# Kernel optimization log

Measured on AMD Instinct MI355X. Metric: run time of the kernel, lower is better.

The kernel has to match this reference:

```python
import jax, jax.numpy as jnp
import numpy as np

C = 512      # input/value channels
DK = 64      # key/query channels (C // 8, SAGAN convention)
N = 4096     # flattened spatial positions (64x64)


def setup_inputs() -> dict:
    key = jax.random.key(0)
    k1, k2, k3, k4 = jax.random.split(key, 4)
    x = jax.random.normal(k1, (C, N), dtype=jnp.float32)
    # 1x1 conv projections == linear maps over the channel dim
    Wk = jax.random.normal(k2, (DK, C), dtype=jnp.float32) * (1.0 / np.sqrt(C))
    Wq = jax.random.normal(k3, (DK, C), dtype=jnp.float32) * (1.0 / np.sqrt(C))
    Wv = jax.random.normal(k4, (C, C), dtype=jnp.float32) * (1.0 / np.sqrt(C))
    return {"x": x, "Wk": Wk, "Wq": Wq, "Wv": Wv}


def reference(x, Wk, Wq, Wv):
    # conv 1x1 projections: [dk, N] / [dk, N] / [C, N]
    kx = Wk @ x
    qx = Wq @ x
    vx = Wv @ x
    # alpha_{i,j} = softmax_j( f(x_i)^T g(x_j) )  -> [N, N]
    scores = jnp.einsum('di,dj->ij', kx, qx)
    attn = jax.nn.softmax(scores, axis=-1)
    # o_i = sum_j alpha_{i,j} h(x_j)  -> [N, C]
    out = attn @ vx.T
    return out
```

## Files before the change

### kernel.cpp

```cpp
#include <hip/hip_runtime.h>
#include <hip/hip_bf16.h>

typedef __bf16 bf16x8 __attribute__((ext_vector_type(8)));
typedef float f32x4 __attribute__((ext_vector_type(4)));
typedef unsigned int u32x4 __attribute__((ext_vector_type(4)));

#define MFMA16(a, b, c) __builtin_amdgcn_mfma_f32_16x16x32_bf16((a), (b), (c), 0, 0, 0)
#define DEVI static __device__ __forceinline__

DEVI unsigned short f2bf(float f) {
  union { float f; unsigned u; } x; x.f = f;
  unsigned r = x.u + 0x7fffu + ((x.u >> 16) & 1u);
  return (unsigned short)(r >> 16);
}
DEVI float bf2f(unsigned short h) {
  union { unsigned u; float f; } x; x.u = ((unsigned)h) << 16;
  return x.f;
}
DEVI bf16x8 ld16(const void* p) {
  u32x4 t = *reinterpret_cast<const u32x4*>(p);
  return __builtin_bit_cast(bf16x8, t);
}

__global__ __launch_bounds__(256) void prep_kernel(
    const float* __restrict__ x,
    const float* __restrict__ Wk, const float* __restrict__ Wq, const float* __restrict__ Wv,
    unsigned short* __restrict__ xThi, unsigned short* __restrict__ xTlo,
    unsigned short* __restrict__ Wkhi, unsigned short* __restrict__ Wklo,
    unsigned short* __restrict__ Wqhi, unsigned short* __restrict__ Wqlo,
    unsigned short* __restrict__ Wvhi, unsigned short* __restrict__ Wvlo) {
  __shared__ float xs[64][65];
  const int bid = blockIdx.x;
  const int t = threadIdx.x;
  if (bid < 512) {
    const int c0 = (bid & 7) * 64, j0 = (bid >> 3) * 64;
    {
      const int cr = t >> 2, jc = (t & 3) * 16;
      const float4* s4 = reinterpret_cast<const float4*>(x + (size_t)(c0 + cr) * 4096 + j0 + jc);
#pragma unroll
      for (int q = 0; q < 4; ++q) {
        float4 v = s4[q];
        xs[cr][jc + q * 4 + 0] = v.x;
        xs[cr][jc + q * 4 + 1] = v.y;
        xs[cr][jc + q * 4 + 2] = v.z;
        xs[cr][jc + q * 4 + 3] = v.w;
      }
    }
    __syncthreads();
    {
      const int jr = t >> 2, cs = (t & 3) * 16;
      unsigned short hb[16] __attribute__((aligned(16)));
      unsigned short lb[16] __attribute__((aligned(16)));
#pragma unroll
      for (int u = 0; u < 16; ++u) {
        float v = xs[cs + u][jr];
        unsigned short h = f2bf(v);
        hb[u] = h;
        lb[u] = f2bf(v - bf2f(h));
      }
      unsigned short* dh = xThi + (size_t)(j0 + jr) * 512 + c0 + cs;
      unsigned short* dl = xTlo + (size_t)(j0 + jr) * 512 + c0 + cs;
      reinterpret_cast<u32x4*>(dh)[0] = reinterpret_cast<const u32x4*>(hb)[0];
      reinterpret_cast<u32x4*>(dh)[1] = reinterpret_cast<const u32x4*>(hb)[1];
      reinterpret_cast<u32x4*>(dl)[0] = reinterpret_cast<const u32x4*>(lb)[0];
      reinterpret_cast<u32x4*>(dl)[1] = reinterpret_cast<const u32x4*>(lb)[1];
    }
  } else {
    const int nk = 64 * 512 / 4, nv = 512 * 512 / 4;
    int i = (bid - 512) * 256 + t;
    const float* in; unsigned short* hi; unsigned short* lo; int idx;
    if (i < nk)               { in = Wk; hi = Wkhi; lo = Wklo; idx = i; }
    else if (i < 2 * nk)      { in = Wq; hi = Wqhi; lo = Wqlo; idx = i - nk; }
    else if (i < 2 * nk + nv) { in = Wv; hi = Wvhi; lo = Wvlo; idx = i - 2 * nk; }
    else return;
    float4 v = reinterpret_cast<const float4*>(in)[idx];
    float vv[4] = {v.x, v.y, v.z, v.w};
    unsigned short hb[4] __attribute__((aligned(8)));
    unsigned short lb[4] __attribute__((aligned(8)));
#pragma unroll
    for (int e = 0; e < 4; ++e) { hb[e] = f2bf(vv[e]); lb[e] = f2bf(vv[e] - bf2f(hb[e])); }
    reinterpret_cast<uint2*>(hi)[idx] = *reinterpret_cast<const uint2*>(hb);
    reinterpret_cast<uint2*>(lo)[idx] = *reinterpret_cast<const uint2*>(lb);
  }
}

__global__ __launch_bounds__(256) void proj_kernel(
    const unsigned short* __restrict__ Wkhi, const unsigned short* __restrict__ Wklo,
    const unsigned short* __restrict__ Wqhi, const unsigned short* __restrict__ Wqlo,
    const unsigned short* __restrict__ Wvhi, const unsigned short* __restrict__ Wvlo,
    const unsigned short* __restrict__ xThi, const unsigned short* __restrict__ xTlo,
    unsigned short* __restrict__ kxThi, unsigned short* __restrict__ kxTlo,
    unsigned short* __restrict__ qxThi, unsigned short* __restrict__ qxTlo,
    unsigned short* __restrict__ vbf) {
  const int y = blockIdx.y;
  const int w = threadIdx.x >> 6, lane = threadIdx.x & 63;
  const int li = lane & 15, g = lane >> 4;
  if (y < 8) {
    const int j0 = blockIdx.x * 64 + (w >> 1) * 32;
    const int c0 = y * 64 + (w & 1) * 32;
    f32x4 acc[2][2];
#pragma unroll
    for (int mf = 0; mf < 2; ++mf)
#pragma unroll
      for (int nf = 0; nf < 2; ++nf) acc[mf][nf] = f32x4{0.f, 0.f, 0.f, 0.f};
    for (int kf = 0; kf < 16; ++kf) {
      const int kk = kf * 32 + g * 8;
      bf16x8 ah[2], al[2], bh[2], bl[2];
#pragma unroll
      for (int mf = 0; mf < 2; ++mf) {
        ah[mf] = ld16(xThi + (size_t)(j0 + mf * 16 + li) * 512 + kk);
        al[mf] = ld16(xTlo + (size_t)(j0 + mf * 16 + li) * 512 + kk);
      }
#pragma unroll
      for (int nf = 0; nf < 2; ++nf) {
        bh[nf] = ld16(Wvhi + (size_t)(c0 + nf * 16 + li) * 512 + kk);
        bl[nf] = ld16(Wvlo + (size_t)(c0 + nf * 16 + li) * 512 + kk);
      }
#pragma unroll
      for (int mf = 0; mf < 2; ++mf)
#pragma unroll
        for (int nf = 0; nf < 2; ++nf) {
          acc[mf][nf] = MFMA16(ah[mf], bh[nf], acc[mf][nf]);
          acc[mf][nf] = MFMA16(ah[mf], bl[nf], acc[mf][nf]);
          acc[mf][nf] = MFMA16(al[mf], bh[nf], acc[mf][nf]);
        }
    }
#pragma unroll
    for (int mf = 0; mf < 2; ++mf)
#pragma unroll
      for (int nf = 0; nf < 2; ++nf) {
        unsigned short hv[4] __attribute__((aligned(8)));
#pragma unroll
        for (int r = 0; r < 4; ++r) hv[r] = f2bf(acc[mf][nf][r]);
        *reinterpret_cast<uint2*>(vbf + (size_t)(c0 + nf * 16 + li) * 4096 + j0 + mf * 16 + g * 4) =
            *reinterpret_cast<const uint2*>(hv);
      }
  } else {
    const int mb = y - 8;
    const int j0 = blockIdx.x * 64 + w * 16;
    const unsigned short* Whi = (mb < 4 ? Wkhi : Wqhi) + (size_t)((mb & 3) * 16 + li) * 512 + g * 8;
    const unsigned short* Wlo = (mb < 4 ? Wklo : Wqlo) + (size_t)((mb & 3) * 16 + li) * 512 + g * 8;
    const unsigned short* Xh = xThi + (size_t)(j0 + li) * 512 + g * 8;
    const unsigned short* Xl = xTlo + (size_t)(j0 + li) * 512 + g * 8;
    f32x4 acc = f32x4{0.f, 0.f, 0.f, 0.f};
    for (int kf = 0; kf < 16; ++kf) {
      const int o = kf * 32;
      bf16x8 ah = ld16(Whi + o), al = ld16(Wlo + o);
      bf16x8 bh = ld16(Xh + o), bl = ld16(Xl + o);
      acc = MFMA16(ah, bh, acc);
      acc = MFMA16(ah, bl, acc);
      acc = MFMA16(al, bh, acc);
    }
    unsigned short hv[4] __attribute__((aligned(8))), lv[4] __attribute__((aligned(8)));
#pragma unroll
    for (int r = 0; r < 4; ++r) {
      hv[r] = f2bf(acc[r]);
      lv[r] = f2bf(acc[r] - bf2f(hv[r]));
    }
    unsigned short* oh = (mb < 4 ? kxThi : qxThi) + (size_t)(j0 + li) * 64 + (mb & 3) * 16 + g * 4;
    unsigned short* ol = (mb < 4 ? kxTlo : qxTlo) + (size_t)(j0 + li) * 64 + (mb & 3) * 16 + g * 4;
    *reinterpret_cast<uint2*>(oh) = *reinterpret_cast<const uint2*>(hv);
    *reinterpret_cast<uint2*>(ol) = *reinterpret_cast<const uint2*>(lv);
  }
}

__global__ __launch_bounds__(256, 2) void attn_kernel(
    const unsigned short* __restrict__ kxThi, const unsigned short* __restrict__ kxTlo,
    const unsigned short* __restrict__ qxThi, const unsigned short* __restrict__ qxTlo,
    const unsigned short* __restrict__ vbf,
    unsigned short* __restrict__ pacc, float* __restrict__ pml, int split) {
  __shared__ __align__(16) unsigned short PL[4096];
  __shared__ __align__(16) float smax[64][4];
  __shared__ __align__(16) float ssum[64][4];
  const int jchunk = 4096 / split;
  const int s = blockIdx.x % split;
  const int i0 = (blockIdx.x / split) * 64;
  const int jbase = s * jchunk;
  const int w = threadIdx.x >> 6, lane = threadIdx.x & 63;
  const int li = lane & 15, g = lane >> 4;
  const float L2E = 1.4426950408889634f;
  char* plb = reinterpret_cast<char*>(PL);

  bf16x8 qh[4][2], ql[4][2];
#pragma unroll
  for (int f = 0; f < 4; ++f)
#pragma unroll
    for (int kf = 0; kf < 2; ++kf) {
      const size_t o = (size_t)(i0 + f * 16 + li) * 64 + kf * 32 + g * 8;
      qh[f][kf] = ld16(kxThi + o);
      ql[f][kf] = ld16(kxTlo + o);
    }
  f32x4 acc[8][4];
#pragma unroll
  for (int cf = 0; cf < 8; ++cf)
#pragma unroll
    for (int f = 0; f < 4; ++f) acc[cf][f] = f32x4{0.f, 0.f, 0.f, 0.f};
  float m_run[4] = {-3.0e38f, -3.0e38f, -3.0e38f, -3.0e38f};
  float l_run[4] = {0.f, 0.f, 0.f, 0.f};

  for (int jj = 0; jj < jchunk; jj += 64) {
    const int j0 = jbase + jj;
    f32x4 sc[4];
#pragma unroll
    for (int f = 0; f < 4; ++f) sc[f] = f32x4{0.f, 0.f, 0.f, 0.f};
    {
      const unsigned short* ah_p = qxThi + (size_t)(j0 + w * 16 + li) * 64 + g * 8;
      const unsigned short* al_p = qxTlo + (size_t)(j0 + w * 16 + li) * 64 + g * 8;
#pragma unroll
      for (int kf = 0; kf < 2; ++kf) {
        bf16x8 ah = ld16(ah_p + kf * 32);
        bf16x8 al = ld16(al_p + kf * 32);
#pragma unroll
        for (int f = 0; f < 4; ++f) {
          sc[f] = MFMA16(ah, qh[f][kf], sc[f]);
          sc[f] = MFMA16(ah, ql[f][kf], sc[f]);
          sc[f] = MFMA16(al, qh[f][kf], sc[f]);
        }
      }
    }
    {
      float pm[4];
#pragma unroll
      for (int f = 0; f < 4; ++f) {
        float tm = fmaxf(fmaxf(sc[f][0], sc[f][1]), fmaxf(sc[f][2], sc[f][3]));
        tm = fmaxf(tm, __shfl_xor(tm, 16));
        tm = fmaxf(tm, __shfl_xor(tm, 32));
        pm[f] = tm;
      }
      if (lane < 16) {
#pragma unroll
        for (int f = 0; f < 4; ++f) smax[f * 16 + li][w] = pm[f];
      }
    }
    __syncthreads();
    float fac[4];
#pragma unroll
    for (int f = 0; f < 4; ++f) {
      const f32x4 sm = *reinterpret_cast<const f32x4*>(&smax[f * 16 + li][0]);
      const float m_new = fmaxf(fmaxf(sm[0], sm[1]), fmaxf(sm[2], sm[3]));
      fac[f] = 1.0f;
      if (m_new > m_run[f] + 8.0f) {
        fac[f] = exp2f((m_run[f] - m_new) * L2E);
        m_run[f] = m_new;
#pragma unroll
        for (int cf = 0; cf < 8; ++cf) {
#pragma unroll
          for (int r = 0; r < 4; ++r) acc[cf][f][r] *= fac[f];
        }
      }
    }
#pragma unroll
    for (int f = 0; f < 4; ++f) {
      float p[4];
#pragma unroll
      for (int r = 0; r < 4; ++r) p[r] = exp2f((sc[f][r] - m_run[f]) * L2E);
      float ps = (p[0] + p[1]) + (p[2] + p[3]);
      ps += __shfl_xor(ps, 16);
      ps += __shfl_xor(ps, 32);
      if (lane < 16) ssum[f * 16 + li][w] = ps;
      unsigned short pv[4] __attribute__((aligned(8)));
#pragma unroll
      for (int r = 0; r < 4; ++r) pv[r] = f2bf(p[r]);
      const int pb = ((f * 16 + li) * 128 + w * 32 + g * 8) ^ ((li & 7) << 4);
      *reinterpret_cast<uint2*>(plb + pb) = *reinterpret_cast<const uint2*>(pv);
    }
    __syncthreads();
#pragma unroll
    for (int f = 0; f < 4; ++f) {
      const f32x4 ss = *reinterpret_cast<const f32x4*>(&ssum[f * 16 + li][0]);
      l_run[f] = l_run[f] * fac[f] + ((ss[0] + ss[1]) + (ss[2] + ss[3]));
    }
    bf16x8 bp[4][2];
#pragma unroll
    for (int f = 0; f < 4; ++f)
#pragma unroll
      for (int kf = 0; kf < 2; ++kf) {
        const int rb = ((f * 16 + li) * 128 + kf * 64 + g * 16) ^ ((li & 7) << 4);
        bp[f][kf] = ld16(plb + rb);
      }
#pragma unroll
    for (int cf = 0; cf < 8; ++cf) {
      const unsigned short* vp = vbf + (size_t)(w * 128 + cf * 16 + li) * 4096 + j0 + g * 8;
      bf16x8 a0 = ld16(vp);
      bf16x8 a1 = ld16(vp + 32);
#pragma unroll
      for (int f = 0; f < 4; ++f) {
        acc[cf][f] = MFMA16(a0, bp[f][0], acc[cf][f]);
        acc[cf][f] = MFMA16(a1, bp[f][1], acc[cf][f]);
      }
    }
  }
#pragma unroll
  for (int cf = 0; cf < 8; ++cf)
#pragma unroll
    for (int f = 0; f < 4; ++f) {
      unsigned short hv[4] __attribute__((aligned(8)));
#pragma unroll
      for (int r = 0; r < 4; ++r) hv[r] = f2bf(acc[cf][f][r]);
      unsigned short* dp = pacc + ((size_t)(s * 4096 + i0 + f * 16 + li)) * 512 + w * 128 + cf * 16 + g * 4;
      *reinterpret_cast<uint2*>(dp) = *reinterpret_cast<const uint2*>(hv);
    }
  if (w == 0 && lane < 16) {
#pragma unroll
    for (int f = 0; f < 4; ++f) {
      pml[((size_t)(s * 4096 + i0 + f * 16 + li)) * 2] = m_run[f];
      pml[((size_t)(s * 4096 + i0 + f * 16 + li)) * 2 + 1] = l_run[f];
    }
  }
}

__global__ __launch_bounds__(256) void combine_kernel(
    const unsigned short* __restrict__ pacc, const float* __restrict__ pml,
    float* __restrict__ out, int split) {
  const int t = blockIdx.x * 256 + threadIdx.x;
  const int i = t >> 6, c8 = (t & 63) << 3;
  const float L2E = 1.4426950408889634f;
  float M = -3.0e38f;
  for (int ss = 0; ss < split; ++ss) M = fmaxf(M, pml[((size_t)ss * 4096 + i) * 2]);
  float num[8];
#pragma unroll
  for (int e = 0; e < 8; ++e) num[e] = 0.f;
  float den = 0.f;
  for (int ss = 0; ss < split; ++ss) {
    const float m = pml[((size_t)ss * 4096 + i) * 2];
    const float l = pml[((size_t)ss * 4096 + i) * 2 + 1];
    const float wgt = exp2f((m - M) * L2E);
    den += wgt * l;
    u32x4 pk = *reinterpret_cast<const u32x4*>(pacc + ((size_t)ss * 4096 + i) * 512 + c8);
#pragma unroll
    for (int e = 0; e < 8; ++e) {
      unsigned short h = (unsigned short)((pk[e >> 1] >> ((e & 1) * 16)) & 0xffffu);
      num[e] += wgt * bf2f(h);
    }
  }
  const float inv = 1.0f / den;
  float4 o0, o1;
  o0.x = num[0] * inv; o0.y = num[1] * inv; o0.z = num[2] * inv; o0.w = num[3] * inv;
  o1.x = num[4] * inv; o1.y = num[5] * inv; o1.z = num[6] * inv; o1.w = num[7] * inv;
  float* op = out + (size_t)i * 512 + c8;
  *reinterpret_cast<float4*>(op) = o0;
  *reinterpret_cast<float4*>(op + 4) = o1;
}

extern "C" void kernel_launch(void* const* d_in, const int* in_sizes, int n_in,
                              void* d_out, int out_size, void* d_ws, size_t ws_size,
                              hipStream_t stream) {
  const float* x  = (const float*)d_in[0];
  const float* Wk = (const float*)d_in[1];
  const float* Wq = (const float*)d_in[2];
  const float* Wv = (const float*)d_in[3];
  float* out = (float*)d_out;
  char* ws = (char*)d_ws;

  const size_t MB = 1024ull * 1024ull;
  const size_t pers_b = 2 * MB  + 4 * MB ;
  int split = 8;
  {
    size_t need8 = (size_t)8 * 4 * MB + 8 * 4096 * 8 + pers_b;
    if (ws_size < need8) split = 4;
  }
  const size_t pacc_b = (size_t)split * 4 * MB;
  const size_t pml_b  = (size_t)split * 4096 * 8;

  char* pers = ws + pacc_b + pml_b;
  unsigned short* pacc  = (unsigned short*)ws;
  float*          pml   = (float*)(ws + pacc_b);
  unsigned short* kxThi = (unsigned short*)(pers + 0 * 512 * 1024);
  unsigned short* kxTlo = (unsigned short*)(pers + 1 * 512 * 1024);
  unsigned short* qxThi = (unsigned short*)(pers + 2 * 512 * 1024);
  unsigned short* qxTlo = (unsigned short*)(pers + 3 * 512 * 1024);
  unsigned short* vbf   = (unsigned short*)(pers + 4 * 512 * 1024);
  unsigned short* xThi = (unsigned short*)(ws + 0 * MB);
  unsigned short* xTlo = (unsigned short*)(ws + 4 * MB);
  char* wbase = ws + 8 * MB;
  unsigned short* Wkhi = (unsigned short*)(wbase + 0 * 64 * 1024);
  unsigned short* Wklo = (unsigned short*)(wbase + 1 * 64 * 1024);
  unsigned short* Wqhi = (unsigned short*)(wbase + 2 * 64 * 1024);
  unsigned short* Wqlo = (unsigned short*)(wbase + 3 * 64 * 1024);
  unsigned short* Wvhi = (unsigned short*)(wbase + 4 * 64 * 1024);
  unsigned short* Wvlo = (unsigned short*)(wbase + 12 * 64 * 1024);
  (void)in_sizes; (void)n_in; (void)out_size;

  hipLaunchKernelGGL(prep_kernel, dim3(512 + 320), dim3(256), 0, stream,
                     x, Wk, Wq, Wv, xThi, xTlo, Wkhi, Wklo, Wqhi, Wqlo, Wvhi, Wvlo);
  hipLaunchKernelGGL(proj_kernel, dim3(64, 16), dim3(256), 0, stream,
                     Wkhi, Wklo, Wqhi, Wqlo, Wvhi, Wvlo, xThi, xTlo,
                     kxThi, kxTlo, qxThi, qxTlo, vbf);
  hipLaunchKernelGGL(attn_kernel, dim3(64 * split), dim3(256), 0, stream,
                     kxThi, kxTlo, qxThi, qxTlo, vbf, pacc, pml, split);
  hipLaunchKernelGGL(combine_kernel, dim3(1024), dim3(256), 0, stream, pacc, pml, out, split);
}
```

Before: 188.2 us.

## Widen attention block to 8 waves, stage K tile in LDS, 128-key steps

The attention kernel now runs 512 threads (8 waves) per block. Each wave owns 64 output channels instead of 128, which halves the accumulator registers, and launch bounds ask for 4 blocks per CU. The block's K/query tile moves from registers into swizzled LDS and is reread every iteration, and each iteration now handles 128 keys. The conditional lazy rescale becomes an unconditional per-step rescale of the accumulators. In exchange it adds LDS traffic and more exponentials and multiplies per step, aiming for higher occupancy and latency hiding.

Result: slower. 229.3 us (+21.8%).

```diff
diff --git a/kernel.cpp b/kernel.cpp
--- a/kernel.cpp
+++ b/kernel.cpp
@@ -164,14 +164,16 @@
   }
 }
 
-__global__ __launch_bounds__(256, 2) void attn_kernel(
+__global__ __launch_bounds__(512, 4) void attn_kernel(
     const unsigned short* __restrict__ kxThi, const unsigned short* __restrict__ kxTlo,
     const unsigned short* __restrict__ qxThi, const unsigned short* __restrict__ qxTlo,
     const unsigned short* __restrict__ vbf,
     unsigned short* __restrict__ pacc, float* __restrict__ pml, int split) {
-  __shared__ __align__(16) unsigned short PL[4096];
-  __shared__ __align__(16) float smax[64][4];
-  __shared__ __align__(16) float ssum[64][4];
+  __shared__ __align__(16) unsigned short QLh[4096];
+  __shared__ __align__(16) unsigned short QLl[4096];
+  __shared__ __align__(16) unsigned short PL[8192];
+  __shared__ __align__(16) float smax[64][8];
+  __shared__ __align__(16) float ssum[64][8];
   const int jchunk = 4096 / split;
   const int s = blockIdx.x % split;
   const int i0 = (blockIdx.x / split) * 64;
@@ -179,26 +181,27 @@
   const int w = threadIdx.x >> 6, lane = threadIdx.x & 63;
   const int li = lane & 15, g = lane >> 4;
   const float L2E = 1.4426950408889634f;
+  char* qlh = reinterpret_cast<char*>(QLh);
+  char* qll = reinterpret_cast<char*>(QLl);
   char* plb = reinterpret_cast<char*>(PL);
 
-  bf16x8 qh[4][2], ql[4][2];
-#pragma unroll
-  for (int f = 0; f < 4; ++f)
-#pragma unroll
-    for (int kf = 0; kf < 2; ++kf) {
-      const size_t o = (size_t)(i0 + f * 16 + li) * 64 + kf * 32 + g * 8;
-      qh[f][kf] = ld16(kxThi + o);
-      ql[f][kf] = ld16(kxTlo + o);
-    }
-  f32x4 acc[8][4];
-#pragma unroll
-  for (int cf = 0; cf < 8; ++cf)
+  {
+    const int row = threadIdx.x >> 3, ch = threadIdx.x & 7;
+    const size_t src = (size_t)(i0 + row) * 64 + ch * 8;
+    const int dst = (row * 128 + ch * 16) ^ ((row & 7) << 4);
+    *reinterpret_cast<u32x4*>(qlh + dst) = *reinterpret_cast<const u32x4*>(kxThi + src);
+    *reinterpret_cast<u32x4*>(qll + dst) = *reinterpret_cast<const u32x4*>(kxTlo + src);
+  }
+  f32x4 acc[4][4];
+#pragma unroll
+  for (int cf = 0; cf < 4; ++cf)
 #pragma unroll
     for (int f = 0; f < 4; ++f) acc[cf][f] = f32x4{0.f, 0.f, 0.f, 0.f};
   float m_run[4] = {-3.0e38f, -3.0e38f, -3.0e38f, -3.0e38f};
   float l_run[4] = {0.f, 0.f, 0.f, 0.f};
-
-  for (int jj = 0; jj < jchunk; jj += 64) {
+  __syncthreads();
+
+  for (int jj = 0; jj < jchunk; jj += 128) {
     const int j0 = jbase + jj;
     f32x4 sc[4];
 #pragma unroll
@@ -212,9 +215,12 @@
         bf16x8 al = ld16(al_p + kf * 32);
 #pragma unroll
         for (int f = 0; f < 4; ++f) {
-          sc[f] = MFMA16(ah, qh[f][kf], sc[f]);
-          sc[f] = MFMA16(ah, ql[f][kf], sc[f]);
-          sc[f] = MFMA16(al, qh[f][kf], sc[f]);
+          const int qb = ((f * 16 + li) * 128 + kf * 64 + g * 16) ^ ((li & 7) << 4);
+          bf16x8 qh = ld16(qlh + qb);
+          bf16x8 ql = ld16(qll + qb);
+          sc[f] = MFMA16(ah, qh, sc[f]);
+          sc[f] = MFMA16(ah, ql, sc[f]);
+          sc[f] = MFMA16(al, qh, sc[f]);
         }
       }
     }
@@ -236,18 +242,13 @@
     float fac[4];
 #pragma unroll
     for (int f = 0; f < 4; ++f) {
-      const f32x4 sm = *reinterpret_cast<const f32x4*>(&smax[f * 16 + li][0]);
-      const float m_new = fmaxf(fmaxf(sm[0], sm[1]), fmaxf(sm[2], sm[3]));
-      fac[f] = 1.0f;
-      if (m_new > m_run[f] + 8.0f) {
-        fac[f] = exp2f((m_run[f] - m_new) * L2E);
-        m_run[f] = m_new;
-#pragma unroll
-        for (int cf = 0; cf < 8; ++cf) {
-#pragma unroll
-          for (int r = 0; r < 4; ++r) acc[cf][f][r] *= fac[f];
-        }
-      }
+      const f32x4 s0 = *reinterpret_cast<const f32x4*>(&smax[f * 16 + li][0]);
+      const f32x4 s1 = *reinterpret_cast<const f32x4*>(&smax[f * 16 + li][4]);
+      const float m_new = fmaxf(m_run[f],
+          fmaxf(fmaxf(fmaxf(s0[0], s0[1]), fmaxf(s0[2], s0[3])),
+                fmaxf(fmaxf(s1[0], s1[1]), fmaxf(s1[2], s1[3]))));
+      fac[f] = exp2f((m_run[f] - m_new) * L2E);
+      m_run[f] = m_new;
     }
 #pragma unroll
     for (int f = 0; f < 4; ++f) {
@@ -261,43 +262,50 @@
       unsigned short pv[4] __attribute__((aligned(8)));
 #pragma unroll
       for (int r = 0; r < 4; ++r) pv[r] = f2bf(p[r]);
-      const int pb = ((f * 16 + li) * 128 + w * 32 + g * 8) ^ ((li & 7) << 4);
+      const int pb = ((f * 16 + li) * 256 + w * 32 + g * 8) ^ ((li & 7) << 4);
       *reinterpret_cast<uint2*>(plb + pb) = *reinterpret_cast<const uint2*>(pv);
     }
     __syncthreads();
 #pragma unroll
     for (int f = 0; f < 4; ++f) {
-      const f32x4 ss = *reinterpret_cast<const f32x4*>(&ssum[f * 16 + li][0]);
-      l_run[f] = l_run[f] * fac[f] + ((ss[0] + ss[1]) + (ss[2] + ss[3]));
-    }
-    bf16x8 bp[4][2];
-#pragma unroll
-    for (int f = 0; f < 4; ++f)
-#pragma unroll
-      for (int kf = 0; kf < 2; ++kf) {
-        const int rb = ((f * 16 + li) * 128 + kf * 64 + g * 16) ^ ((li & 7) << 4);
-        bp[f][kf] = ld16(plb + rb);
-      }
-#pragma unroll
-    for (int cf = 0; cf < 8; ++cf) {
-      const unsigned short* vp = vbf + (size_t)(w * 128 + cf * 16 + li) * 4096 + j0 + g * 8;
-      bf16x8 a0 = ld16(vp);
-      bf16x8 a1 = ld16(vp + 32);
+      const f32x4 s0 = *reinterpret_cast<const f32x4*>(&ssum[f * 16 + li][0]);
+      const f32x4 s1 = *reinterpret_cast<const f32x4*>(&ssum[f * 16 + li][4]);
+      l_run[f] = l_run[f] * fac[f] +
+          (((s0[0] + s0[1]) + (s0[2] + s0[3])) + ((s1[0] + s1[1]) + (s1[2] + s1[3])));
+    }
+#pragma unroll
+    for (int cf = 0; cf < 4; ++cf)
 #pragma unroll
       for (int f = 0; f < 4; ++f) {
-        acc[cf][f] = MFMA16(a0, bp[f][0], acc[cf][f]);
-        acc[cf][f] = MFMA16(a1, bp[f][1], acc[cf][f]);
-      }
-    }
-  }
-#pragma unroll
-  for (int cf = 0; cf < 8; ++cf)
+#pragma unroll
+        for (int r = 0; r < 4; ++r) acc[cf][f][r] *= fac[f];
+      }
+#pragma unroll
+    for (int kf = 0; kf < 4; ++kf) {
+      bf16x8 bpf[4];
+#pragma unroll
+      for (int f = 0; f < 4; ++f) {
+        const int rb = ((f * 16 + li) * 256 + kf * 64 + g * 16) ^ ((li & 7) << 4);
+        bpf[f] = ld16(plb + rb);
+      }
+#pragma unroll
+      for (int cf = 0; cf < 4; ++cf) {
+        const unsigned short* vp =
+            vbf + (size_t)(w * 64 + cf * 16 + li) * 4096 + j0 + kf * 32 + g * 8;
+        bf16x8 a = ld16(vp);
+#pragma unroll
+        for (int f = 0; f < 4; ++f) acc[cf][f] = MFMA16(a, bpf[f], acc[cf][f]);
+      }
+    }
+  }
+#pragma unroll
+  for (int cf = 0; cf < 4; ++cf)
 #pragma unroll
     for (int f = 0; f < 4; ++f) {
       unsigned short hv[4] __attribute__((aligned(8)));
 #pragma unroll
       for (int r = 0; r < 4; ++r) hv[r] = f2bf(acc[cf][f][r]);
-      unsigned short* dp = pacc + ((size_t)(s * 4096 + i0 + f * 16 + li)) * 512 + w * 128 + cf * 16 + g * 4;
+      unsigned short* dp = pacc + ((size_t)(s * 4096 + i0 + f * 16 + li)) * 512 + w * 64 + cf * 16 + g * 4;
       *reinterpret_cast<uint2*>(dp) = *reinterpret_cast<const uint2*>(hv);
     }
   if (w == 0 && lane < 16) {
@@ -386,7 +394,7 @@
   hipLaunchKernelGGL(proj_kernel, dim3(64, 16), dim3(256), 0, stream,
                      Wkhi, Wklo, Wqhi, Wqlo, Wvhi, Wvlo, xThi, xTlo,
                      kxThi, kxTlo, qxThi, qxTlo, vbf);
-  hipLaunchKernelGGL(attn_kernel, dim3(64 * split), dim3(256), 0, stream,
+  hipLaunchKernelGGL(attn_kernel, dim3(64 * split), dim3(512), 0, stream,
                      kxThi, kxTlo, qxThi, qxTlo, vbf, pacc, pml, split);
   hipLaunchKernelGGL(combine_kernel, dim3(1024), dim3(256), 0, stream, pacc, pml, out, split);
 }
```

## Stage query fragments in LDS, rescale accumulators unconditionally, raise split to 16

Applied to the files above, without the earlier changes.

Query hi/lo fragments now sit in swizzled shared memory and are reloaded per MFMA instead of being held in 32 VGPRs. This frees registers for the 256-thread, 2-block launch bound. The lazy rescale threshold is replaced by an unconditional online-softmax rescale of all accumulators every tile. The split-K factor rises to 16 when the workspace allows, for more blocks and parallelism. The cost is extra LDS reads, more multiplies per tile, and a larger partial-combine pass.

New measurement: 186.5 us. No clear change (-0.9%).

```diff
diff --git a/kernel.cpp b/kernel.cpp
--- a/kernel.cpp
+++ b/kernel.cpp
@@ -169,6 +169,8 @@
     const unsigned short* __restrict__ qxThi, const unsigned short* __restrict__ qxTlo,
     const unsigned short* __restrict__ vbf,
     unsigned short* __restrict__ pacc, float* __restrict__ pml, int split) {
+  __shared__ __align__(16) unsigned short QLh[4096];
+  __shared__ __align__(16) unsigned short QLl[4096];
   __shared__ __align__(16) unsigned short PL[4096];
   __shared__ __align__(16) float smax[64][4];
   __shared__ __align__(16) float ssum[64][4];
@@ -179,17 +181,21 @@
   const int w = threadIdx.x >> 6, lane = threadIdx.x & 63;
   const int li = lane & 15, g = lane >> 4;
   const float L2E = 1.4426950408889634f;
+  char* qlh = reinterpret_cast<char*>(QLh);
+  char* qll = reinterpret_cast<char*>(QLl);
   char* plb = reinterpret_cast<char*>(PL);
 
-  bf16x8 qh[4][2], ql[4][2];
-#pragma unroll
-  for (int f = 0; f < 4; ++f)
-#pragma unroll
-    for (int kf = 0; kf < 2; ++kf) {
-      const size_t o = (size_t)(i0 + f * 16 + li) * 64 + kf * 32 + g * 8;
-      qh[f][kf] = ld16(kxThi + o);
-      ql[f][kf] = ld16(kxTlo + o);
-    }
+  {
+    const int qi = threadIdx.x >> 2;
+#pragma unroll
+    for (int cc = 0; cc < 2; ++cc) {
+      const int ch = (threadIdx.x & 3) + cc * 4;
+      const size_t src = (size_t)(i0 + qi) * 64 + ch * 8;
+      const int dst = (qi * 128 + ch * 16) ^ ((qi & 7) << 4);
+      *reinterpret_cast<u32x4*>(qlh + dst) = *reinterpret_cast<const u32x4*>(kxThi + src);
+      *reinterpret_cast<u32x4*>(qll + dst) = *reinterpret_cast<const u32x4*>(kxTlo + src);
+    }
+  }
   f32x4 acc[8][4];
 #pragma unroll
   for (int cf = 0; cf < 8; ++cf)
@@ -197,6 +203,7 @@
     for (int f = 0; f < 4; ++f) acc[cf][f] = f32x4{0.f, 0.f, 0.f, 0.f};
   float m_run[4] = {-3.0e38f, -3.0e38f, -3.0e38f, -3.0e38f};
   float l_run[4] = {0.f, 0.f, 0.f, 0.f};
+  __syncthreads();
 
   for (int jj = 0; jj < jchunk; jj += 64) {
     const int j0 = jbase + jj;
@@ -212,9 +219,12 @@
         bf16x8 al = ld16(al_p + kf * 32);
 #pragma unroll
         for (int f = 0; f < 4; ++f) {
-          sc[f] = MFMA16(ah, qh[f][kf], sc[f]);
-          sc[f] = MFMA16(ah, ql[f][kf], sc[f]);
-          sc[f] = MFMA16(al, qh[f][kf], sc[f]);
+          const int qb = ((f * 16 + li) * 128 + kf * 64 + g * 16) ^ ((li & 7) << 4);
+          bf16x8 qh = ld16(qlh + qb);
+          bf16x8 ql = ld16(qll + qb);
+          sc[f] = MFMA16(ah, qh, sc[f]);
+          sc[f] = MFMA16(ah, ql, sc[f]);
+          sc[f] = MFMA16(al, qh, sc[f]);
         }
       }
     }
@@ -237,17 +247,9 @@
 #pragma unroll
     for (int f = 0; f < 4; ++f) {
       const f32x4 sm = *reinterpret_cast<const f32x4*>(&smax[f * 16 + li][0]);
-      const float m_new = fmaxf(fmaxf(sm[0], sm[1]), fmaxf(sm[2], sm[3]));
-      fac[f] = 1.0f;
-      if (m_new > m_run[f] + 8.0f) {
-        fac[f] = exp2f((m_run[f] - m_new) * L2E);
-        m_run[f] = m_new;
-#pragma unroll
-        for (int cf = 0; cf < 8; ++cf) {
-#pragma unroll
-          for (int r = 0; r < 4; ++r) acc[cf][f][r] *= fac[f];
-        }
-      }
+      const float m_new = fmaxf(m_run[f], fmaxf(fmaxf(sm[0], sm[1]), fmaxf(sm[2], sm[3])));
+      fac[f] = exp2f((m_run[f] - m_new) * L2E);
+      m_run[f] = m_new;
     }
 #pragma unroll
     for (int f = 0; f < 4; ++f) {
@@ -270,6 +272,13 @@
       const f32x4 ss = *reinterpret_cast<const f32x4*>(&ssum[f * 16 + li][0]);
       l_run[f] = l_run[f] * fac[f] + ((ss[0] + ss[1]) + (ss[2] + ss[3]));
     }
+#pragma unroll
+    for (int cf = 0; cf < 8; ++cf)
+#pragma unroll
+      for (int f = 0; f < 4; ++f) {
+#pragma unroll
+        for (int r = 0; r < 4; ++r) acc[cf][f][r] *= fac[f];
+      }
     bf16x8 bp[4][2];
 #pragma unroll
     for (int f = 0; f < 4; ++f)
@@ -354,10 +363,12 @@
 
   const size_t MB = 1024ull * 1024ull;
   const size_t pers_b = 2 * MB  + 4 * MB ;
-  int split = 8;
+  int split = 16;
   {
-    size_t need8 = (size_t)8 * 4 * MB + 8 * 4096 * 8 + pers_b;
-    if (ws_size < need8) split = 4;
+    size_t need16 = (size_t)16 * 4 * MB + (size_t)16 * 4096 * 8 + pers_b;
+    size_t need8  = (size_t)8  * 4 * MB + (size_t)8  * 4096 * 8 + pers_b;
+    if (ws_size < need16) split = 8;
+    if (ws_size < need8)  split = 4;
   }
   const size_t pacc_b = (size_t)split * 4 * MB;
   const size_t pml_b  = (size_t)split * 4096 * 8;
```
